# Performance work log

Hardware: AMD Instinct MI355X
Metric: run time of the kernel (lower is better)

## Reference

```python
import jax, jax.numpy as jnp
import numpy as np

N_HEAD, D_MODEL, D_HEAD = 16, 1024, 64
SCALE = 1.0 / (D_HEAD ** 0.5)
LN_EPS = 1e-5


def _rel_shift(x):
    # x: [b, n, i, j] -> Transformer-XL relative shift
    b, n, i, j = x.shape
    zero_pad = jnp.zeros((b, n, i, 1), x.dtype)
    x_padded = jnp.concatenate([zero_pad, x], axis=3).reshape(b, n, j + 1, i)
    return x_padded[:, :, 1:, :].reshape(b, n, i, j)


def setup_inputs() -> dict:
    key = jax.random.key(0)
    ks = jax.random.split(key, 16)
    qlen, bsz, mem_len = 1024, 2, 1024
    klen = qlen + mem_len
    rlen = klen
    s = 0.02
    inp = {
        'w': jax.random.normal(ks[0], (qlen, bsz, D_MODEL), jnp.float32),
        'r': jax.random.normal(ks[1], (rlen, D_MODEL), jnp.float32),
        'mems': jax.random.normal(ks[2], (mem_len, bsz, D_MODEL), jnp.float32),
        'r_w_bias': s * jax.random.normal(ks[3], (N_HEAD, D_HEAD), jnp.float32),
        'r_r_bias': s * jax.random.normal(ks[4], (N_HEAD, D_HEAD), jnp.float32),
        # causal mask with memory offset: position i attends to j <= i + mem_len
        'attn_mask': jnp.triu(jnp.ones((qlen, klen), bool), k=1 + mem_len),
        'Wq': s * jax.random.normal(ks[5], (D_MODEL, N_HEAD * D_HEAD), jnp.float32),
        'bq': jnp.zeros((N_HEAD * D_HEAD,), jnp.float32),
        'Wk': s * jax.random.normal(ks[6], (D_MODEL, N_HEAD * D_HEAD), jnp.float32),
        'bk': jnp.zeros((N_HEAD * D_HEAD,), jnp.float32),
        'Wv': s * jax.random.normal(ks[7], (D_MODEL, N_HEAD * D_HEAD), jnp.float32),
        'bv': jnp.zeros((N_HEAD * D_HEAD,), jnp.float32),
        'Wr': s * jax.random.normal(ks[8], (D_MODEL, N_HEAD * D_HEAD), jnp.float32),
        'br': jnp.zeros((N_HEAD * D_HEAD,), jnp.float32),
        'Wo': s * jax.random.normal(ks[9], (N_HEAD * D_HEAD, D_MODEL), jnp.float32),
        'bo': jnp.zeros((D_MODEL,), jnp.float32),
        'ln_g': jnp.ones((D_MODEL,), jnp.float32),
        'ln_b': jnp.zeros((D_MODEL,), jnp.float32),
    }
    return inp


def reference(w, r, mems, r_w_bias, r_r_bias, Wq, bq, Wk, bk, Wv, bv, Wr, br, Wo, bo, ln_g, ln_b, attn_mask):
    qlen, bsz, _ = w.shape
    cat = jnp.concatenate([mems, w], axis=0)                      # [klen, b, d_model]
    klen = cat.shape[0]
    q = (cat @ Wq + bq)[-qlen:].reshape(qlen, bsz, N_HEAD, D_HEAD)
    k = (cat @ Wk + bk).reshape(klen, bsz, N_HEAD, D_HEAD)
    v = (cat @ Wv + bv).reshape(klen, bsz, N_HEAD, D_HEAD)
    rk = (r @ Wr + br).reshape(-1, N_HEAD, D_HEAD)               # [rlen, n, d]

    AC = jnp.einsum('ibnd,jbnd->bnij', q + r_w_bias, k)          # content term
    BD = _rel_shift(jnp.einsum('ibnd,jnd->bnij', q + r_r_bias, rk))  # relative term
    attn_score = SCALE * (AC + BD)                                # [b, n, i, j]
    attn_score = jnp.where(attn_mask[None, None, :, :], -jnp.inf, attn_score)
    attn_prob = jax.nn.softmax(attn_score, axis=3)
    attn_vec = jnp.einsum('bnij,jbnd->ibnd', attn_prob, v).reshape(qlen, bsz, N_HEAD * D_HEAD)
    attn_out = attn_vec @ Wo + bo

    res = w + attn_out                                            # post-LN (pre_lnorm=False)
    mu = jnp.mean(res, axis=-1, keepdims=True)
    var = jnp.var(res, axis=-1, keepdims=True)
    return (res - mu) / jnp.sqrt(var + LN_EPS) * ln_g + ln_b
```

## Files before the change

### kernel.cpp

```cpp
#include <hip/hip_runtime.h>
#include <math.h>

#define N_HEADC 16
#define D_MODELC 1024
#define D_HEADC 64
#define QLENC 1024
#define BSZC 2
#define MEMLENC 1024
#define KLENC 2048
#define SCALEC 0.125f
#define SL2C 0.18033688011112042f
#define LN_EPSC 1e-5f
#define RINGC 192

typedef __attribute__((ext_vector_type(8))) short short8;
typedef __attribute__((ext_vector_type(4))) float f32x4;

#define MFMA16(a, b, c) __builtin_amdgcn_mfma_f32_16x16x32_bf16((a), (b), (c), 0, 0, 0)

__device__ inline unsigned short f2bf(float x) {
    union { float f; unsigned int u; } c; c.f = x;
    unsigned int r = c.u + 0x7FFFu + ((c.u >> 16) & 1u);
    return (unsigned short)(r >> 16);
}
__device__ inline unsigned int pk2(float a, float b) {
    union { float f; unsigned int u; } x, y; x.f = a; y.f = b;
    return (x.u >> 16) | (y.u & 0xFFFF0000u);
}
__device__ inline float bf2f(short s) {
    union { unsigned int u; float f; } c; c.u = ((unsigned int)(unsigned short)s) << 16;
    return c.f;
}

__device__ __forceinline__ void load_lds16(const short* g, short* l) {
    __builtin_amdgcn_global_load_lds(
        (const __attribute__((address_space(1))) void*)g,
        (__attribute__((address_space(3))) void*)l,
        16, 0, 0);
}

__global__ __launch_bounds__(256) void cast_cat_kernel(
    const float* __restrict__ s0, const float* __restrict__ s1, int splitElems,
    short* __restrict__ dst)
{
    int idx = (blockIdx.x * 256 + threadIdx.x) * 8;
    const float* src = (idx < splitElems) ? (s0 + idx) : (s1 + (idx - splitElems));
    short8 o;
    #pragma unroll
    for (int e = 0; e < 8; ++e) o[e] = (short)f2bf(src[e]);
    *(short8*)(dst + idx) = o;
}

__global__ __launch_bounds__(256) void tcast5_kernel(
    const float* __restrict__ W0, const float* __restrict__ W1,
    const float* __restrict__ W2, const float* __restrict__ W3,
    const float* __restrict__ W4,
    short* __restrict__ D0, short* __restrict__ D1, short* __restrict__ D2,
    short* __restrict__ D3, short* __restrict__ D4)
{
    __shared__ short tile[64][72];
    const float* W; short* D;
    switch (blockIdx.z) {
        case 0: W = W0; D = D0; break;
        case 1: W = W1; D = D1; break;
        case 2: W = W2; D = D2; break;
        case 3: W = W3; D = D3; break;
        default: W = W4; D = D4; break;
    }
    const int t = threadIdx.x;
    const int n0 = blockIdx.x * 64, k0 = blockIdx.y * 64;
    #pragma unroll
    for (int it = 0; it < 2; ++it) {
        int idx = t + it * 256;
        int kl = idx >> 3, c8 = idx & 7;
        const float* src = W + (size_t)(k0 + kl) * D_MODELC + n0 + c8 * 8;
        short8 s;
        #pragma unroll
        for (int e = 0; e < 8; ++e) s[e] = (short)f2bf(src[e]);
        *(short8*)&tile[kl][c8 * 8] = s;
    }
    __syncthreads();
    #pragma unroll
    for (int it = 0; it < 2; ++it) {
        int idx = t + it * 256;
        int nl = idx >> 3, c8 = idx & 7;
        short8 s;
        #pragma unroll
        for (int e = 0; e < 8; ++e) s[e] = tile[c8 * 8 + e][nl];
        *(short8*)(D + (size_t)(n0 + nl) * D_MODELC + k0 + c8 * 8) = s;
    }
}

__global__ __launch_bounds__(256) void vtrans_kernel(
    const short* __restrict__ v_bf, short* __restrict__ vt)
{
    __shared__ short tile[64][72];
    const int t = threadIdx.x;
    const int j0 = blockIdx.x * 64;
    const int bn = blockIdx.y;
    const int b = bn & 1, n = bn >> 1;
    #pragma unroll
    for (int it = 0; it < 2; ++it) {
        int idx = t + it * 256;
        int jl = idx >> 3, c8 = idx & 7;
        short8 s = *(const short8*)(v_bf + ((size_t)(j0 + jl) * 2 + b) * D_MODELC + n * 64 + c8 * 8);
        *(short8*)&tile[jl][c8 * 8] = s;
    }
    __syncthreads();
    #pragma unroll
    for (int it = 0; it < 2; ++it) {
        int idx = t + it * 256;
        int dl = idx >> 3, c8 = idx & 7;
        short8 s;
        #pragma unroll
        for (int e = 0; e < 8; ++e) s[e] = tile[c8 * 8 + e][dl];
        *(short8*)(vt + ((size_t)(b * 16 + n) * 64 + dl) * (size_t)KLENC + j0 + c8 * 8) = s;
    }
}

__global__ __launch_bounds__(256, 3) void proj_gemm_kernel(
    const short* __restrict__ cat, const short* __restrict__ rin,
    const short* __restrict__ WqT, const short* __restrict__ WkT,
    const short* __restrict__ WvT, const short* __restrict__ WrT,
    const float* __restrict__ bq, const float* __restrict__ bk,
    const float* __restrict__ bv, const float* __restrict__ br,
    const float* __restrict__ rwb, const float* __restrict__ rrb,
    short* __restrict__ qw, short* __restrict__ qr,
    short* __restrict__ kb, short* __restrict__ vb, short* __restrict__ rk)
{
    __shared__ short As[128][32];
    __shared__ short Bs[128][32];

    const int lin = blockIdx.y * 8 + blockIdx.x;
    const int sw  = (lin & 7) * 96 + (lin >> 3);
    const int bx  = sw & 7;
    const int by  = sw >> 3;

    const short* A; const short* Bt; const float* bias; int yt, mode;
    if (by < 32)      { A = cat;                         Bt = WkT; bias = bk; yt = by;      mode = 0; }
    else if (by < 64) { A = cat;                         Bt = WvT; bias = bv; yt = by - 32; mode = 1; }
    else if (by < 80) { A = cat + (size_t)2048 * 1024;   Bt = WqT; bias = bq; yt = by - 64; mode = 2; }
    else              { A = rin;                         Bt = WrT; bias = br; yt = by - 80; mode = 3; }

    const int row0 = yt * 128, col0 = bx * 128;
    const int t = threadIdx.x;
    const int lane = t & 63, wid = t >> 6;
    const int row16 = lane & 15, g8 = lane >> 4;
    const int wr = wid >> 1, wc = wid & 1;

    f32x4 acc[4][4];
    #pragma unroll
    for (int m = 0; m < 4; ++m)
        #pragma unroll
        for (int nn = 0; nn < 4; ++nn)
            acc[m][nn] = (f32x4){0.f, 0.f, 0.f, 0.f};

    short* AsB = &As[0][0] + wid * 1024;
    short* BsB = &Bs[0][0] + wid * 1024;
    const int srow4 = lane >> 2;
    const int cs4 = (lane & 3) ^ ((lane >> 3) & 3);
    const short* Ag = A  + (size_t)(row0 + wid * 32 + srow4) * D_MODELC + cs4 * 8;
    const short* Bg = Bt + (size_t)(col0 + wid * 32 + srow4) * D_MODELC + cs4 * 8;
    const int xc2 = (row16 >> 1) & 3;

    for (int k0 = 0; k0 < D_MODELC; k0 += 32) {
        load_lds16(Ag + k0,              AsB);
        load_lds16(Ag + k0 + 16 * 1024,  AsB + 512);
        load_lds16(Bg + k0,              BsB);
        load_lds16(Bg + k0 + 16 * 1024,  BsB + 512);
        __syncthreads();
        short8 af[4], bfr[4];
        #pragma unroll
        for (int m = 0; m < 4; ++m)
            af[m] = *(const short8*)&As[wr * 64 + m * 16 + row16][(g8 ^ xc2) * 8];
        #pragma unroll
        for (int nn = 0; nn < 4; ++nn)
            bfr[nn] = *(const short8*)&Bs[wc * 64 + nn * 16 + row16][(g8 ^ xc2) * 8];
        #pragma unroll
        for (int m = 0; m < 4; ++m)
            #pragma unroll
            for (int nn = 0; nn < 4; ++nn)
                acc[m][nn] = MFMA16(af[m], bfr[nn], acc[m][nn]);
        __syncthreads();
    }

    float bvv[4], w1[4], w2[4];
    #pragma unroll
    for (int nn = 0; nn < 4; ++nn) {
        int c = col0 + wc * 64 + nn * 16 + row16;
        bvv[nn] = bias[c];
        w1[nn] = rwb[c];
        w2[nn] = rrb[c];
    }
    if (mode == 2) {
        #pragma unroll
        for (int m = 0; m < 4; ++m)
            #pragma unroll
            for (int nn = 0; nn < 4; ++nn) {
                int c = col0 + wc * 64 + nn * 16 + row16;
                #pragma unroll
                for (int reg = 0; reg < 4; ++reg) {
                    int r = row0 + wr * 64 + m * 16 + g8 * 4 + reg;
                    float v = acc[m][nn][reg] + bvv[nn];
                    qw[(size_t)r * D_MODELC + c] = (short)f2bf(v + w1[nn]);
                    qr[(size_t)r * D_MODELC + c] = (short)f2bf(v + w2[nn]);
                }
            }
    } else {
        short* C = (mode == 0) ? kb : (mode == 1) ? vb : rk;
        #pragma unroll
        for (int m = 0; m < 4; ++m)
            #pragma unroll
            for (int nn = 0; nn < 4; ++nn) {
                int c = col0 + wc * 64 + nn * 16 + row16;
                #pragma unroll
                for (int reg = 0; reg < 4; ++reg) {
                    int r = row0 + wr * 64 + m * 16 + g8 * 4 + reg;
                    C[(size_t)r * D_MODELC + c] = (short)f2bf(acc[m][nn][reg] + bvv[nn]);
                }
            }
    }
}

__global__ __launch_bounds__(256, 3) void wo_gemm_kernel(
    const short* __restrict__ A, const short* __restrict__ Bt,
    float* __restrict__ out0, float* __restrict__ out1)
{
    __shared__ short As[128][32];
    __shared__ short Bs[128][32];
    const int kz = blockIdx.z;
    float* C = kz ? out1 : out0;
    const int row0 = blockIdx.y * 128, col0 = blockIdx.x * 128;
    const int t = threadIdx.x;
    const int lane = t & 63, wid = t >> 6;
    const int row16 = lane & 15, g8 = lane >> 4;
    const int wr = wid >> 1, wc = wid & 1;

    f32x4 acc[4][4];
    #pragma unroll
    for (int m = 0; m < 4; ++m)
        #pragma unroll
        for (int nn = 0; nn < 4; ++nn)
            acc[m][nn] = (f32x4){0.f, 0.f, 0.f, 0.f};

    short* AsB = &As[0][0] + wid * 1024;
    short* BsB = &Bs[0][0] + wid * 1024;
    const int srow4 = lane >> 2;
    const int cs4 = (lane & 3) ^ ((lane >> 3) & 3);
    const short* Ag = A  + (size_t)(row0 + wid * 32 + srow4) * D_MODELC + cs4 * 8;
    const short* Bg = Bt + (size_t)(col0 + wid * 32 + srow4) * D_MODELC + cs4 * 8;
    const int xc2 = (row16 >> 1) & 3;

    const int kbase = kz * 512;
    for (int k0 = kbase; k0 < kbase + 512; k0 += 32) {
        load_lds16(Ag + k0,             AsB);
        load_lds16(Ag + k0 + 16 * 1024, AsB + 512);
        load_lds16(Bg + k0,             BsB);
        load_lds16(Bg + k0 + 16 * 1024, BsB + 512);
        __syncthreads();
        short8 af[4], bfr[4];
        #pragma unroll
        for (int m = 0; m < 4; ++m)
            af[m] = *(const short8*)&As[wr * 64 + m * 16 + row16][(g8 ^ xc2) * 8];
        #pragma unroll
        for (int nn = 0; nn < 4; ++nn)
            bfr[nn] = *(const short8*)&Bs[wc * 64 + nn * 16 + row16][(g8 ^ xc2) * 8];
        #pragma unroll
        for (int m = 0; m < 4; ++m)
            #pragma unroll
            for (int nn = 0; nn < 4; ++nn)
                acc[m][nn] = MFMA16(af[m], bfr[nn], acc[m][nn]);
        __syncthreads();
    }

    #pragma unroll
    for (int m = 0; m < 4; ++m)
        #pragma unroll
        for (int nn = 0; nn < 4; ++nn) {
            int c = col0 + wc * 64 + nn * 16 + row16;
            #pragma unroll
            for (int reg = 0; reg < 4; ++reg) {
                int r = row0 + wr * 64 + m * 16 + g8 * 4 + reg;
                C[(size_t)r * D_MODELC + c] = acc[m][nn][reg];
            }
        }
}

__global__ __launch_bounds__(256, 2) void attn_mfma_kernel(
    const short* __restrict__ qw, const short* __restrict__ qr,
    const short* __restrict__ kb, const short* __restrict__ rkb,
    const short* __restrict__ vt, short* __restrict__ av)
{
    __shared__ short Kl[2][64][64];
    __shared__ short Vl[2][64][64];
    __shared__ short Rl[RINGC][64];
    __shared__ short pun[4][1376];
    __shared__ float scb[4][16];

    const int wave = threadIdx.x >> 6, lane = threadIdx.x & 63;
    const int row16 = lane & 15, g8 = lane >> 4;
    const int srow = lane >> 3, chk = lane & 7;
    const int swz = srow & 7;

    const int lin = blockIdx.y * 16 + blockIdx.x;
    const int xcd = lin & 7;
    const int u   = lin >> 3;
    const int v   = u & 31;
    const int bn  = xcd * 4 + (v >> 3);
    const int tt  = v & 7;
    const int ic  = (u >> 5) ? (15 - tt) : tt;
    const int b = bn & 1, n = bn >> 1;
    const int i0 = ic * 64;
    const int i0w = i0 + wave * 16;

    short8 qwf[2], qrf[2];
    #pragma unroll
    for (int ks = 0; ks < 2; ++ks) {
        size_t off = ((size_t)(i0w + row16) * 2 + b) * D_MODELC + n * 64 + ks * 32 + g8 * 8;
        qwf[ks] = *(const short8*)(qw + off);
        qrf[ks] = *(const short8*)(qr + off);
    }

    #pragma unroll
    for (int t = 0; t < 2; ++t) {
        int rr = wave * 16 + t * 8;
        int j  = rr + srow;
        int cs = chk ^ swz;
        load_lds16(kb + ((size_t)j * 2 + b) * D_MODELC + n * 64 + cs * 8, &Kl[0][rr][0]);
        load_lds16(vt + ((size_t)((b * 16 + n) * 64 + rr + srow)) * KLENC + cs * 8,
                   &Vl[0][rr][0]);
    }
    {
        const int p0 = 960 - i0;
        #pragma unroll
        for (int t = 0; t < 4; ++t) {
            int jrb_ = p0 + wave * 32 + t * 8;
            int slotb = jrb_ % RINGC;
            int jr = jrb_ + srow;
            int jc = jr < KLENC ? jr : KLENC - 1;
            int cs = chk ^ swz;
            load_lds16(rkb + (size_t)jc * D_MODELC + n * 64 + cs * 8, &Rl[slotb][0]);
        }
    }

    f32x4 accO[4];
    #pragma unroll
    for (int dt = 0; dt < 4; ++dt) accO[dt] = (f32x4){0.f, 0.f, 0.f, 0.f};
    float m = -INFINITY, lsum = 0.f;

    const int T = (i0 + 63 + MEMLENC + 64) >> 6;
    const int r7 = row16 & 7;

    __syncthreads();

    int cur = 0;
    for (int s = 0; s < T; ++s) {
        const int j0 = s * 64;
        const int nxt = cur ^ 1;

        #pragma unroll
        for (int t = 0; t < 2; ++t) {
            int rr = wave * 16 + t * 8;
            int j  = j0 + 64 + rr + srow;
            if (j > KLENC - 1) j = KLENC - 1;
            int cs = chk ^ swz;
            load_lds16(kb + ((size_t)j * 2 + b) * D_MODELC + n * 64 + cs * 8, &Kl[nxt][rr][0]);
        }
        {
            const int nb = j0 + 1088 - i0;
            #pragma unroll
            for (int t = 0; t < 2; ++t) {
                int jrb_ = nb + wave * 16 + t * 8;
                int slotb = jrb_ % RINGC;
                int jr = jrb_ + srow;
                int jc = jr < KLENC ? jr : KLENC - 1;
                int cs = chk ^ swz;
                load_lds16(rkb + (size_t)jc * D_MODELC + n * 64 + cs * 8, &Rl[slotb][0]);
            }
        }
        {
            const int jsrc = (j0 + 64 <= KLENC - 64) ? (j0 + 64) : (KLENC - 64);
            #pragma unroll
            for (int t = 0; t < 2; ++t) {
                int rr = wave * 16 + t * 8;
                int cs = chk ^ swz;
                load_lds16(vt + ((size_t)((b * 16 + n) * 64 + rr + srow)) * KLENC + jsrc + cs * 8,
                           &Vl[nxt][rr][0]);
            }
        }

        __builtin_amdgcn_s_setprio(1);
        f32x4 st[4];
        #pragma unroll
        for (int jt = 0; jt < 4; ++jt) {
            st[jt] = (f32x4){0.f, 0.f, 0.f, 0.f};
            const short* kr = &Kl[cur][jt * 16 + row16][0];
            st[jt] = MFMA16(*(const short8*)(kr + ((g8 ^ r7) * 8)),       qwf[0], st[jt]);
            st[jt] = MFMA16(*(const short8*)(kr + (((4 + g8) ^ r7) * 8)), qwf[1], st[jt]);
        }

        const int jrb_w = j0 - i0w + 1008;
        const int sb = jrb_w % RINGC;
        short* bdT = &pun[wave][0];
        #pragma unroll
        for (int rt = 0; rt < 5; ++rt) {
            int rsl = sb + rt * 16 + row16;
            if (rsl >= RINGC) rsl -= RINGC;
            const short* rr = &Rl[rsl][0];
            f32x4 bd = (f32x4){0.f, 0.f, 0.f, 0.f};
            bd = MFMA16(*(const short8*)(rr + ((g8 ^ r7) * 8)),       qrf[0], bd);
            bd = MFMA16(*(const short8*)(rr + (((4 + g8) ^ r7) * 8)), qrf[1], bd);
            uint2 wv;
            wv.x = pk2(bd[0], bd[1]);
            wv.y = pk2(bd[2], bd[3]);
            *(uint2*)&bdT[row16 * 84 + rt * 16 + g8 * 4] = wv;
        }
        __builtin_amdgcn_s_setprio(0);

        float sl[4][4];
        #pragma unroll
        for (int jt = 0; jt < 4; ++jt)
            #pragma unroll
            for (int reg = 0; reg < 4; ++reg) {
                const int jl = jt * 16 + g8 * 4 + reg;
                float vv = st[jt][reg] + bf2f(bdT[row16 * 84 + jl + 15 - row16]);
                sl[jt][reg] = (j0 + jl > i0w + row16 + MEMLENC) ? -INFINITY : vv * SL2C;
            }

        float mx0 = fmaxf(fmaxf(sl[0][0], sl[0][1]), fmaxf(sl[0][2], sl[0][3]));
        float mx1 = fmaxf(fmaxf(sl[1][0], sl[1][1]), fmaxf(sl[1][2], sl[1][3]));
        float mx2 = fmaxf(fmaxf(sl[2][0], sl[2][1]), fmaxf(sl[2][2], sl[2][3]));
        float mx3 = fmaxf(fmaxf(sl[3][0], sl[3][1]), fmaxf(sl[3][2], sl[3][3]));
        float mx = fmaxf(fmaxf(mx0, mx1), fmaxf(mx2, mx3));
        mx = fmaxf(mx, __shfl_xor(mx, 16, 64));
        mx = fmaxf(mx, __shfl_xor(mx, 32, 64));

        if (__any(mx > m + 8.f)) {
            float mn = fmaxf(m, mx);
            float sc = exp2f(m - mn);
            m = mn;
            lsum *= sc;
            if (lane < 16) scb[wave][lane] = sc;
            float4 s4 = *(const float4*)&scb[wave][g8 * 4];
            #pragma unroll
            for (int dt = 0; dt < 4; ++dt) {
                accO[dt][0] *= s4.x; accO[dt][1] *= s4.y;
                accO[dt][2] *= s4.z; accO[dt][3] *= s4.w;
            }
        }

        float ps = 0.f;
        #pragma unroll
        for (int jt = 0; jt < 4; ++jt)
            #pragma unroll
            for (int reg = 0; reg < 4; ++reg) {
                float p = exp2f(sl[jt][reg] - m);
                sl[jt][reg] = p;
                ps += p;
            }
        short* pP = &pun[wave][0];
        #pragma unroll
        for (int jt = 0; jt < 4; ++jt) {
            const int ch = (jt * 2 + (g8 >> 1)) ^ r7;
            uint2 pkd;
            pkd.x = pk2(sl[jt][0], sl[jt][1]);
            pkd.y = pk2(sl[jt][2], sl[jt][3]);
            *(uint2*)&pP[row16 * 64 + ch * 8 + (g8 & 1) * 4] = pkd;
        }
        ps += __shfl_xor(ps, 16, 64);
        ps += __shfl_xor(ps, 32, 64);
        lsum += ps;

        __builtin_amdgcn_s_setprio(1);
        #pragma unroll
        for (int ks2 = 0; ks2 < 2; ++ks2) {
            short8 pf = *(const short8*)&pP[row16 * 64 + (((ks2 * 4 + g8) ^ r7) * 8)];
            #pragma unroll
            for (int dt = 0; dt < 4; ++dt) {
                const short* vp = &Vl[cur][dt * 16 + row16][(((ks2 * 4 + g8) ^ r7) * 8)];
                accO[dt] = MFMA16(pf, *(const short8*)vp, accO[dt]);
            }
        }
        __builtin_amdgcn_s_setprio(0);

        __syncthreads();
        cur = nxt;
    }

    if (lane < 16) scb[wave][lane] = lsum;
    float4 l4 = *(const float4*)&scb[wave][g8 * 4];
    float rl4[4] = {1.f / l4.x, 1.f / l4.y, 1.f / l4.z, 1.f / l4.w};
    #pragma unroll
    for (int dt = 0; dt < 4; ++dt)
        #pragma unroll
        for (int reg = 0; reg < 4; ++reg) {
            size_t o = ((size_t)(i0w + g8 * 4 + reg) * 2 + b) * D_MODELC + n * 64 + dt * 16 + row16;
            av[o] = (short)f2bf(accO[dt][reg] * rl4[reg]);
        }
}

__global__ __launch_bounds__(256) void ln_kernel(
    const float* __restrict__ w, const float* __restrict__ ao0,
    const float* __restrict__ ao1, const float* __restrict__ bo,
    const float* __restrict__ g, const float* __restrict__ bb,
    float* __restrict__ out)
{
    __shared__ float red[2][4];
    const int row = blockIdx.x;
    const int lane = threadIdx.x & 63;
    const int wv = threadIdx.x >> 6;
    const size_t base = (size_t)row * D_MODELC;
    const int c = threadIdx.x * 4;

    float4 xw = *(const float4*)&w[base + c];
    float4 x0 = *(const float4*)&ao0[base + c];
    float4 x1 = *(const float4*)&ao1[base + c];
    float4 xb = *(const float4*)&bo[c];
    float x[4] = {xw.x + x0.x + x1.x + xb.x, xw.y + x0.y + x1.y + xb.y,
                  xw.z + x0.z + x1.z + xb.z, xw.w + x0.w + x1.w + xb.w};

    float sum = x[0] + x[1] + x[2] + x[3];
    float ssq = x[0]*x[0] + x[1]*x[1] + x[2]*x[2] + x[3]*x[3];
    #pragma unroll
    for (int off = 32; off > 0; off >>= 1) {
        sum += __shfl_xor(sum, off, 64);
        ssq += __shfl_xor(ssq, off, 64);
    }
    if (lane == 0) { red[0][wv] = sum; red[1][wv] = ssq; }
    __syncthreads();
    sum = red[0][0] + red[0][1] + red[0][2] + red[0][3];
    ssq = red[1][0] + red[1][1] + red[1][2] + red[1][3];

    const float mu = sum * (1.0f / D_MODELC);
    const float var = ssq * (1.0f / D_MODELC) - mu * mu;
    const float rstd = rsqrtf(var + LN_EPSC);

    float4 o;
    o.x = (x[0] - mu) * rstd * g[c] + bb[c];
    o.y = (x[1] - mu) * rstd * g[c+1] + bb[c+1];
    o.z = (x[2] - mu) * rstd * g[c+2] + bb[c+2];
    o.w = (x[3] - mu) * rstd * g[c+3] + bb[c+3];
    *(float4*)&out[base + c] = o;
}

extern "C" void kernel_launch(void* const* d_in, const int* in_sizes, int n_in,
                              void* d_out, int out_size, void* d_ws, size_t ws_size,
                              hipStream_t stream)
{
    const float* w    = (const float*)d_in[0];
    const float* r    = (const float*)d_in[1];
    const float* mems = (const float*)d_in[2];
    const float* rwb  = (const float*)d_in[3];
    const float* rrb  = (const float*)d_in[4];
    const float* Wq = (const float*)d_in[6];
    const float* bq = (const float*)d_in[7];
    const float* Wk = (const float*)d_in[8];
    const float* bk = (const float*)d_in[9];
    const float* Wv = (const float*)d_in[10];
    const float* bv = (const float*)d_in[11];
    const float* Wr = (const float*)d_in[12];
    const float* br = (const float*)d_in[13];
    const float* Wo = (const float*)d_in[14];
    const float* bo = (const float*)d_in[15];
    const float* ln_g = (const float*)d_in[16];
    const float* ln_b = (const float*)d_in[17];
    float* out = (float*)d_out;

    char* ws = (char*)d_ws;
    const size_t MB = 1ull << 20;
    short* cat_bf = (short*)(ws + 0 * MB);
    short* r_bf   = (short*)(ws + 8 * MB);
    short* Wq_t   = (short*)(ws + 12 * MB);
    short* Wk_t   = (short*)(ws + 14 * MB);
    short* Wv_t   = (short*)(ws + 16 * MB);
    short* Wr_t   = (short*)(ws + 18 * MB);
    short* Wo_t   = (short*)(ws + 20 * MB);
    short* qw_bf  = (short*)(ws + 22 * MB);
    short* qr_bf  = (short*)(ws + 26 * MB);
    short* k_bf   = (short*)(ws + 30 * MB);
    short* v_bf   = (short*)(ws + 38 * MB);
    short* rk_bf  = (short*)(ws + 46 * MB);
    short* vt     = (short*)(ws + 50 * MB);
    short* av_bf  = (short*)(ws + 58 * MB);
    float* ao0    = (float*)v_bf;
    float* ao1    = (float*)k_bf;

    dim3 blk(256);

    cast_cat_kernel<<<dim3(2048), blk, 0, stream>>>(mems, w, 2048 * 1024, cat_bf);
    cast_cat_kernel<<<dim3(1024), blk, 0, stream>>>(r, r, 1 << 30, r_bf);

    tcast5_kernel<<<dim3(16, 16, 5), blk, 0, stream>>>(
        Wq, Wk, Wv, Wr, Wo, Wq_t, Wk_t, Wv_t, Wr_t, Wo_t);

    proj_gemm_kernel<<<dim3(8, 96), blk, 0, stream>>>(
        cat_bf, r_bf, Wq_t, Wk_t, Wv_t, Wr_t,
        bq, bk, bv, br, rwb, rrb,
        qw_bf, qr_bf, k_bf, v_bf, rk_bf);

    vtrans_kernel<<<dim3(32, 32), blk, 0, stream>>>(v_bf, vt);

    attn_mfma_kernel<<<dim3(16, 32), blk, 0, stream>>>(
        qw_bf, qr_bf, k_bf, rk_bf, vt, av_bf);

    wo_gemm_kernel<<<dim3(8, 16, 2), blk, 0, stream>>>(av_bf, Wo_t, ao0, ao1);

    ln_kernel<<<dim3(2048), blk, 0, stream>>>(w, ao0, ao1, bo, ln_g, ln_b, out);
}
```

Measured before the change: 156.5 us.

## Triple-buffer GEMM k-loops, defer PV matmul, fold softmax scale into Q

The projection and output GEMMs now use a three-stage LDS ring with prefetch two tiles ahead. A vmcnt wait plus a single barrier replaces the two __syncthreads per k-step, and the MFMA block runs at raised priority. The attention kernel adds a third V buffer and software-pipelines P·V: the previous tile's P·V runs while the next tile's scores are computed. It also pre-multiplies Q by the log2 softmax scale in the projection epilogue, and skips masking on tiles that are fully unmasked. The cost is more LDS per block, which may reduce occupancy, and the reordered P/bdT buffer reuse carries some correctness risk.

New measurement: 159.3 us. About the same (+1.8%).

```diff
diff --git a/kernel.cpp b/kernel.cpp
--- a/kernel.cpp
+++ b/kernel.cpp
@@ -128,8 +128,8 @@
     short* __restrict__ qw, short* __restrict__ qr,
     short* __restrict__ kb, short* __restrict__ vb, short* __restrict__ rk)
 {
-    __shared__ short As[128][32];
-    __shared__ short Bs[128][32];
+    __shared__ short As[3][128][32];
+    __shared__ short Bs[3][128][32];
 
     const int lin = blockIdx.y * 8 + blockIdx.x;
     const int sw  = (lin & 7) * 96 + (lin >> 3);
@@ -155,34 +155,51 @@
         for (int nn = 0; nn < 4; ++nn)
             acc[m][nn] = (f32x4){0.f, 0.f, 0.f, 0.f};
 
-    short* AsB = &As[0][0] + wid * 1024;
-    short* BsB = &Bs[0][0] + wid * 1024;
     const int srow4 = lane >> 2;
     const int cs4 = (lane & 3) ^ ((lane >> 3) & 3);
     const short* Ag = A  + (size_t)(row0 + wid * 32 + srow4) * D_MODELC + cs4 * 8;
     const short* Bg = Bt + (size_t)(col0 + wid * 32 + srow4) * D_MODELC + cs4 * 8;
     const int xc2 = (row16 >> 1) & 3;
 
-    for (int k0 = 0; k0 < D_MODELC; k0 += 32) {
-        load_lds16(Ag + k0,              AsB);
-        load_lds16(Ag + k0 + 16 * 1024,  AsB + 512);
-        load_lds16(Bg + k0,              BsB);
-        load_lds16(Bg + k0 + 16 * 1024,  BsB + 512);
-        __syncthreads();
+    #pragma unroll
+    for (int pb = 0; pb < 2; ++pb) {
+        int k0 = pb * 32;
+        load_lds16(Ag + k0,             &As[pb][0][0] + wid * 1024);
+        load_lds16(Ag + k0 + 16 * 1024, &As[pb][0][0] + wid * 1024 + 512);
+        load_lds16(Bg + k0,             &Bs[pb][0][0] + wid * 1024);
+        load_lds16(Bg + k0 + 16 * 1024, &Bs[pb][0][0] + wid * 1024 + 512);
+    }
+    asm volatile("s_waitcnt vmcnt(4)" ::: "memory");
+    __builtin_amdgcn_s_barrier();
+
+    for (int kk = 0; kk < 32; ++kk) {
+        int kpre = (kk + 2 <= 31) ? (kk + 2) * 32 : 31 * 32;
+        int bpre = (kk + 2) % 3;
+        load_lds16(Ag + kpre,             &As[bpre][0][0] + wid * 1024);
+        load_lds16(Ag + kpre + 16 * 1024, &As[bpre][0][0] + wid * 1024 + 512);
+        load_lds16(Bg + kpre,             &Bs[bpre][0][0] + wid * 1024);
+        load_lds16(Bg + kpre + 16 * 1024, &Bs[bpre][0][0] + wid * 1024 + 512);
+
+        const int bc = kk % 3;
         short8 af[4], bfr[4];
         #pragma unroll
         for (int m = 0; m < 4; ++m)
-            af[m] = *(const short8*)&As[wr * 64 + m * 16 + row16][(g8 ^ xc2) * 8];
+            af[m] = *(const short8*)&As[bc][wr * 64 + m * 16 + row16][(g8 ^ xc2) * 8];
         #pragma unroll
         for (int nn = 0; nn < 4; ++nn)
-            bfr[nn] = *(const short8*)&Bs[wc * 64 + nn * 16 + row16][(g8 ^ xc2) * 8];
+            bfr[nn] = *(const short8*)&Bs[bc][wc * 64 + nn * 16 + row16][(g8 ^ xc2) * 8];
+        __builtin_amdgcn_s_setprio(1);
         #pragma unroll
         for (int m = 0; m < 4; ++m)
             #pragma unroll
             for (int nn = 0; nn < 4; ++nn)
                 acc[m][nn] = MFMA16(af[m], bfr[nn], acc[m][nn]);
-        __syncthreads();
-    }
+        __builtin_amdgcn_s_setprio(0);
+
+        asm volatile("s_waitcnt vmcnt(4)" ::: "memory");
+        __builtin_amdgcn_s_barrier();
+    }
+    asm volatile("s_waitcnt vmcnt(0)" ::: "memory");
 
     float bvv[4], w1[4], w2[4];
     #pragma unroll
@@ -202,8 +219,8 @@
                 for (int reg = 0; reg < 4; ++reg) {
                     int r = row0 + wr * 64 + m * 16 + g8 * 4 + reg;
                     float v = acc[m][nn][reg] + bvv[nn];
-                    qw[(size_t)r * D_MODELC + c] = (short)f2bf(v + w1[nn]);
-                    qr[(size_t)r * D_MODELC + c] = (short)f2bf(v + w2[nn]);
+                    qw[(size_t)r * D_MODELC + c] = (short)f2bf((v + w1[nn]) * SL2C);
+                    qr[(size_t)r * D_MODELC + c] = (short)f2bf((v + w2[nn]) * SL2C);
                 }
             }
     } else {
@@ -226,8 +243,8 @@
     const short* __restrict__ A, const short* __restrict__ Bt,
     float* __restrict__ out0, float* __restrict__ out1)
 {
-    __shared__ short As[128][32];
-    __shared__ short Bs[128][32];
+    __shared__ short As[3][128][32];
+    __shared__ short Bs[3][128][32];
     const int kz = blockIdx.z;
     float* C = kz ? out1 : out0;
     const int row0 = blockIdx.y * 128, col0 = blockIdx.x * 128;
@@ -243,35 +260,52 @@
         for (int nn = 0; nn < 4; ++nn)
             acc[m][nn] = (f32x4){0.f, 0.f, 0.f, 0.f};
 
-    short* AsB = &As[0][0] + wid * 1024;
-    short* BsB = &Bs[0][0] + wid * 1024;
     const int srow4 = lane >> 2;
     const int cs4 = (lane & 3) ^ ((lane >> 3) & 3);
-    const short* Ag = A  + (size_t)(row0 + wid * 32 + srow4) * D_MODELC + cs4 * 8;
-    const short* Bg = Bt + (size_t)(col0 + wid * 32 + srow4) * D_MODELC + cs4 * 8;
+    const int kbase = kz * 512;
+    const short* Ag = A  + (size_t)(row0 + wid * 32 + srow4) * D_MODELC + kbase + cs4 * 8;
+    const short* Bg = Bt + (size_t)(col0 + wid * 32 + srow4) * D_MODELC + kbase + cs4 * 8;
     const int xc2 = (row16 >> 1) & 3;
 
-    const int kbase = kz * 512;
-    for (int k0 = kbase; k0 < kbase + 512; k0 += 32) {
-        load_lds16(Ag + k0,             AsB);
-        load_lds16(Ag + k0 + 16 * 1024, AsB + 512);
-        load_lds16(Bg + k0,             BsB);
-        load_lds16(Bg + k0 + 16 * 1024, BsB + 512);
-        __syncthreads();
+    #pragma unroll
+    for (int pb = 0; pb < 2; ++pb) {
+        int k0 = pb * 32;
+        load_lds16(Ag + k0,             &As[pb][0][0] + wid * 1024);
+        load_lds16(Ag + k0 + 16 * 1024, &As[pb][0][0] + wid * 1024 + 512);
+        load_lds16(Bg + k0,             &Bs[pb][0][0] + wid * 1024);
+        load_lds16(Bg + k0 + 16 * 1024, &Bs[pb][0][0] + wid * 1024 + 512);
+    }
+    asm volatile("s_waitcnt vmcnt(4)" ::: "memory");
+    __builtin_amdgcn_s_barrier();
+
+    for (int kk = 0; kk < 16; ++kk) {
+        int kpre = (kk + 2 <= 15) ? (kk + 2) * 32 : 15 * 32;
+        int bpre = (kk + 2) % 3;
+        load_lds16(Ag + kpre,             &As[bpre][0][0] + wid * 1024);
+        load_lds16(Ag + kpre + 16 * 1024, &As[bpre][0][0] + wid * 1024 + 512);
+        load_lds16(Bg + kpre,             &Bs[bpre][0][0] + wid * 1024);
+        load_lds16(Bg + kpre + 16 * 1024, &Bs[bpre][0][0] + wid * 1024 + 512);
+
+        const int bc = kk % 3;
         short8 af[4], bfr[4];
         #pragma unroll
         for (int m = 0; m < 4; ++m)
-            af[m] = *(const short8*)&As[wr * 64 + m * 16 + row16][(g8 ^ xc2) * 8];
+            af[m] = *(const short8*)&As[bc][wr * 64 + m * 16 + row16][(g8 ^ xc2) * 8];
         #pragma unroll
         for (int nn = 0; nn < 4; ++nn)
-            bfr[nn] = *(const short8*)&Bs[wc * 64 + nn * 16 + row16][(g8 ^ xc2) * 8];
+            bfr[nn] = *(const short8*)&Bs[bc][wc * 64 + nn * 16 + row16][(g8 ^ xc2) * 8];
+        __builtin_amdgcn_s_setprio(1);
         #pragma unroll
         for (int m = 0; m < 4; ++m)
             #pragma unroll
             for (int nn = 0; nn < 4; ++nn)
                 acc[m][nn] = MFMA16(af[m], bfr[nn], acc[m][nn]);
-        __syncthreads();
-    }
+        __builtin_amdgcn_s_setprio(0);
+
+        asm volatile("s_waitcnt vmcnt(4)" ::: "memory");
+        __builtin_amdgcn_s_barrier();
+    }
+    asm volatile("s_waitcnt vmcnt(0)" ::: "memory");
 
     #pragma unroll
     for (int m = 0; m < 4; ++m)
@@ -292,7 +326,7 @@
     const short* __restrict__ vt, short* __restrict__ av)
 {
     __shared__ short Kl[2][64][64];
-    __shared__ short Vl[2][64][64];
+    __shared__ short Vl[3][64][64];
     __shared__ short Rl[RINGC][64];
     __shared__ short pun[4][1376];
     __shared__ float scb[4][16];
@@ -354,6 +388,7 @@
     __syncthreads();
 
     int cur = 0;
+    int vp = 2, vc = 0, vn = 1;
     for (int s = 0; s < T; ++s) {
         const int j0 = s * 64;
         const int nxt = cur ^ 1;
@@ -385,9 +420,12 @@
                 int rr = wave * 16 + t * 8;
                 int cs = chk ^ swz;
                 load_lds16(vt + ((size_t)((b * 16 + n) * 64 + rr + srow)) * KLENC + jsrc + cs * 8,
-                           &Vl[nxt][rr][0]);
-            }
-        }
+                           &Vl[vn][rr][0]);
+            }
+        }
+
+        short* pP  = &pun[wave][0];
+        short* bdT = &pun[wave][0];
 
         __builtin_amdgcn_s_setprio(1);
         f32x4 st[4];
@@ -399,9 +437,20 @@
             st[jt] = MFMA16(*(const short8*)(kr + (((4 + g8) ^ r7) * 8)), qwf[1], st[jt]);
         }
 
+        if (s) {
+            #pragma unroll
+            for (int ks2 = 0; ks2 < 2; ++ks2) {
+                short8 pf = *(const short8*)&pP[row16 * 64 + (((ks2 * 4 + g8) ^ r7) * 8)];
+                #pragma unroll
+                for (int dt = 0; dt < 4; ++dt) {
+                    const short* vpp = &Vl[vp][dt * 16 + row16][(((ks2 * 4 + g8) ^ r7) * 8)];
+                    accO[dt] = MFMA16(pf, *(const short8*)vpp, accO[dt]);
+                }
+            }
+        }
+
         const int jrb_w = j0 - i0w + 1008;
         const int sb = jrb_w % RINGC;
-        short* bdT = &pun[wave][0];
         #pragma unroll
         for (int rt = 0; rt < 5; ++rt) {
             int rsl = sb + rt * 16 + row16;
@@ -418,14 +467,24 @@
         __builtin_amdgcn_s_setprio(0);
 
         float sl[4][4];
-        #pragma unroll
-        for (int jt = 0; jt < 4; ++jt)
-            #pragma unroll
-            for (int reg = 0; reg < 4; ++reg) {
-                const int jl = jt * 16 + g8 * 4 + reg;
-                float vv = st[jt][reg] + bf2f(bdT[row16 * 84 + jl + 15 - row16]);
-                sl[jt][reg] = (j0 + jl > i0w + row16 + MEMLENC) ? -INFINITY : vv * SL2C;
-            }
+        if (j0 + 63 <= i0w + MEMLENC) {
+            #pragma unroll
+            for (int jt = 0; jt < 4; ++jt)
+                #pragma unroll
+                for (int reg = 0; reg < 4; ++reg) {
+                    const int jl = jt * 16 + g8 * 4 + reg;
+                    sl[jt][reg] = st[jt][reg] + bf2f(bdT[row16 * 84 + jl + 15 - row16]);
+                }
+        } else {
+            #pragma unroll
+            for (int jt = 0; jt < 4; ++jt)
+                #pragma unroll
+                for (int reg = 0; reg < 4; ++reg) {
+                    const int jl = jt * 16 + g8 * 4 + reg;
+                    float vv = st[jt][reg] + bf2f(bdT[row16 * 84 + jl + 15 - row16]);
+                    sl[jt][reg] = (j0 + jl > i0w + row16 + MEMLENC) ? -INFINITY : vv;
+                }
+        }
 
         float mx0 = fmaxf(fmaxf(sl[0][0], sl[0][1]), fmaxf(sl[0][2], sl[0][3]));
         float mx1 = fmaxf(fmaxf(sl[1][0], sl[1][1]), fmaxf(sl[1][2], sl[1][3]));
@@ -449,16 +508,15 @@
             }
         }
 
-        float ps = 0.f;
         #pragma unroll
         for (int jt = 0; jt < 4; ++jt)
             #pragma unroll
-            for (int reg = 0; reg < 4; ++reg) {
-                float p = exp2f(sl[jt][reg] - m);
-                sl[jt][reg] = p;
-                ps += p;
-            }
-        short* pP = &pun[wave][0];
+            for (int reg = 0; reg < 4; ++reg)
+                sl[jt][reg] = exp2f(sl[jt][reg] - m);
+        float ps = ((sl[0][0] + sl[0][1]) + (sl[0][2] + sl[0][3]))
+                 + ((sl[1][0] + sl[1][1]) + (sl[1][2] + sl[1][3]))
+                 + ((sl[2][0] + sl[2][1]) + (sl[2][2] + sl[2][3]))
+                 + ((sl[3][0] + sl[3][1]) + (sl[3][2] + sl[3][3]));
         #pragma unroll
         for (int jt = 0; jt < 4; ++jt) {
             const int ch = (jt * 2 + (g8 >> 1)) ^ r7;
@@ -471,20 +529,22 @@
         ps += __shfl_xor(ps, 32, 64);
         lsum += ps;
 
-        __builtin_amdgcn_s_setprio(1);
+        __syncthreads();
+        cur = nxt;
+        int tmp = vp; vp = vc; vc = vn; vn = tmp;
+    }
+
+    {
+        short* pP = &pun[wave][0];
         #pragma unroll
         for (int ks2 = 0; ks2 < 2; ++ks2) {
             short8 pf = *(const short8*)&pP[row16 * 64 + (((ks2 * 4 + g8) ^ r7) * 8)];
             #pragma unroll
             for (int dt = 0; dt < 4; ++dt) {
-                const short* vp = &Vl[cur][dt * 16 + row16][(((ks2 * 4 + g8) ^ r7) * 8)];
-                accO[dt] = MFMA16(pf, *(const short8*)vp, accO[dt]);
-            }
-        }
-        __builtin_amdgcn_s_setprio(0);
-
-        __syncthreads();
-        cur = nxt;
+                const short* vpp = &Vl[vp][dt * 16 + row16][(((ks2 * 4 + g8) ^ r7) * 8)];
+                accO[dt] = MFMA16(pf, *(const short8*)vpp, accO[dt]);
+            }
+        }
     }
 
     if (lane < 16) scb[wave][lane] = lsum;
```

## Merge prep casts, fold softmax scale into Q, stream V from global, bf16 Wo partials

Applied to the files above, without the earlier changes.

The three input/weight cast launches become one prep kernel, which cuts launch overhead. The softmax scale is folded into the Q projection epilogue, and masking is skipped for tiles that lie fully in the unmasked region. V fragments are read directly from global memory into registers instead of being staged through LDS. The Wo split-K partials are stored in bf16 to halve their traffic, and setprio is added around the MFMA loops of the GEMMs. These trade some precision (scaled Q in bf16, bf16 partial sums) and global-load latency in the attention loop for less LDS use and less memory traffic.

Measured after the change: 175.2 us. 11.9% more time.

```diff
diff --git a/kernel.cpp b/kernel.cpp
--- a/kernel.cpp
+++ b/kernel.cpp
@@ -39,35 +39,46 @@
         16, 0, 0);
 }
 
-__global__ __launch_bounds__(256) void cast_cat_kernel(
-    const float* __restrict__ s0, const float* __restrict__ s1, int splitElems,
-    short* __restrict__ dst)
-{
-    int idx = (blockIdx.x * 256 + threadIdx.x) * 8;
-    const float* src = (idx < splitElems) ? (s0 + idx) : (s1 + (idx - splitElems));
-    short8 o;
-    #pragma unroll
-    for (int e = 0; e < 8; ++e) o[e] = (short)f2bf(src[e]);
-    *(short8*)(dst + idx) = o;
-}
-
-__global__ __launch_bounds__(256) void tcast5_kernel(
+__global__ __launch_bounds__(256) void prep_kernel(
+    const float* __restrict__ mems, const float* __restrict__ wIn,
+    const float* __restrict__ rIn,
     const float* __restrict__ W0, const float* __restrict__ W1,
     const float* __restrict__ W2, const float* __restrict__ W3,
     const float* __restrict__ W4,
+    short* __restrict__ cat_bf, short* __restrict__ r_bf,
     short* __restrict__ D0, short* __restrict__ D1, short* __restrict__ D2,
     short* __restrict__ D3, short* __restrict__ D4)
 {
     __shared__ short tile[64][72];
+    const int z = blockIdx.z;
+    const int t = threadIdx.x;
+
+    if (z >= 5) {
+        int lb = (z - 5) * 256 + blockIdx.y * 16 + blockIdx.x;
+        int idx = (lb * 256 + t) * 8;
+        const float* src; short* dst;
+        if (idx < 4194304) {
+            src = (idx < 2097152) ? (mems + idx) : (wIn + idx - 2097152);
+            dst = cat_bf + idx;
+        } else {
+            src = rIn + (idx - 4194304);
+            dst = r_bf + (idx - 4194304);
+        }
+        short8 o;
+        #pragma unroll
+        for (int e = 0; e < 8; ++e) o[e] = (short)f2bf(src[e]);
+        *(short8*)dst = o;
+        return;
+    }
+
     const float* W; short* D;
-    switch (blockIdx.z) {
+    switch (z) {
         case 0: W = W0; D = D0; break;
         case 1: W = W1; D = D1; break;
         case 2: W = W2; D = D2; break;
         case 3: W = W3; D = D3; break;
         default: W = W4; D = D4; break;
     }
-    const int t = threadIdx.x;
     const int n0 = blockIdx.x * 64, k0 = blockIdx.y * 64;
     #pragma unroll
     for (int it = 0; it < 2; ++it) {
@@ -176,11 +187,13 @@
         #pragma unroll
         for (int nn = 0; nn < 4; ++nn)
             bfr[nn] = *(const short8*)&Bs[wc * 64 + nn * 16 + row16][(g8 ^ xc2) * 8];
+        __builtin_amdgcn_s_setprio(1);
         #pragma unroll
         for (int m = 0; m < 4; ++m)
             #pragma unroll
             for (int nn = 0; nn < 4; ++nn)
                 acc[m][nn] = MFMA16(af[m], bfr[nn], acc[m][nn]);
+        __builtin_amdgcn_s_setprio(0);
         __syncthreads();
     }
 
@@ -202,8 +215,8 @@
                 for (int reg = 0; reg < 4; ++reg) {
                     int r = row0 + wr * 64 + m * 16 + g8 * 4 + reg;
                     float v = acc[m][nn][reg] + bvv[nn];
-                    qw[(size_t)r * D_MODELC + c] = (short)f2bf(v + w1[nn]);
-                    qr[(size_t)r * D_MODELC + c] = (short)f2bf(v + w2[nn]);
+                    qw[(size_t)r * D_MODELC + c] = (short)f2bf((v + w1[nn]) * SL2C);
+                    qr[(size_t)r * D_MODELC + c] = (short)f2bf((v + w2[nn]) * SL2C);
                 }
             }
     } else {
@@ -224,12 +237,12 @@
 
 __global__ __launch_bounds__(256, 3) void wo_gemm_kernel(
     const short* __restrict__ A, const short* __restrict__ Bt,
-    float* __restrict__ out0, float* __restrict__ out1)
+    short* __restrict__ out0, short* __restrict__ out1)
 {
     __shared__ short As[128][32];
     __shared__ short Bs[128][32];
     const int kz = blockIdx.z;
-    float* C = kz ? out1 : out0;
+    short* C = kz ? out1 : out0;
     const int row0 = blockIdx.y * 128, col0 = blockIdx.x * 128;
     const int t = threadIdx.x;
     const int lane = t & 63, wid = t >> 6;
@@ -251,7 +264,7 @@
     const short* Bg = Bt + (size_t)(col0 + wid * 32 + srow4) * D_MODELC + cs4 * 8;
     const int xc2 = (row16 >> 1) & 3;
 
-    const int kbase = kz * 512;
+    const int kbase = blockIdx.z * 512;
     for (int k0 = kbase; k0 < kbase + 512; k0 += 32) {
         load_lds16(Ag + k0,             AsB);
         load_lds16(Ag + k0 + 16 * 1024, AsB + 512);
@@ -265,11 +278,13 @@
         #pragma unroll
         for (int nn = 0; nn < 4; ++nn)
             bfr[nn] = *(const short8*)&Bs[wc * 64 + nn * 16 + row16][(g8 ^ xc2) * 8];
+        __builtin_amdgcn_s_setprio(1);
         #pragma unroll
         for (int m = 0; m < 4; ++m)
             #pragma unroll
             for (int nn = 0; nn < 4; ++nn)
                 acc[m][nn] = MFMA16(af[m], bfr[nn], acc[m][nn]);
+        __builtin_amdgcn_s_setprio(0);
         __syncthreads();
     }
 
@@ -281,7 +296,7 @@
             #pragma unroll
             for (int reg = 0; reg < 4; ++reg) {
                 int r = row0 + wr * 64 + m * 16 + g8 * 4 + reg;
-                C[(size_t)r * D_MODELC + c] = acc[m][nn][reg];
+                C[(size_t)r * D_MODELC + c] = (short)f2bf(acc[m][nn][reg]);
             }
         }
 }
@@ -292,7 +307,6 @@
     const short* __restrict__ vt, short* __restrict__ av)
 {
     __shared__ short Kl[2][64][64];
-    __shared__ short Vl[2][64][64];
     __shared__ short Rl[RINGC][64];
     __shared__ short pun[4][1376];
     __shared__ float scb[4][16];
@@ -321,14 +335,14 @@
         qrf[ks] = *(const short8*)(qr + off);
     }
 
+    const short* vbase = vt + ((size_t)((b * 16 + n) * 64 + row16)) * KLENC;
+
     #pragma unroll
     for (int t = 0; t < 2; ++t) {
         int rr = wave * 16 + t * 8;
         int j  = rr + srow;
         int cs = chk ^ swz;
         load_lds16(kb + ((size_t)j * 2 + b) * D_MODELC + n * 64 + cs * 8, &Kl[0][rr][0]);
-        load_lds16(vt + ((size_t)((b * 16 + n) * 64 + rr + srow)) * KLENC + cs * 8,
-                   &Vl[0][rr][0]);
     }
     {
         const int p0 = 960 - i0;
@@ -358,6 +372,14 @@
         const int j0 = s * 64;
         const int nxt = cur ^ 1;
 
+        short8 vf[2][4];
+        #pragma unroll
+        for (int ks2 = 0; ks2 < 2; ++ks2)
+            #pragma unroll
+            for (int dt = 0; dt < 4; ++dt)
+                vf[ks2][dt] = *(const short8*)(vbase + (size_t)(dt * 16) * KLENC
+                                               + j0 + ks2 * 32 + g8 * 8);
+
         #pragma unroll
         for (int t = 0; t < 2; ++t) {
             int rr = wave * 16 + t * 8;
@@ -376,16 +398,6 @@
                 int jc = jr < KLENC ? jr : KLENC - 1;
                 int cs = chk ^ swz;
                 load_lds16(rkb + (size_t)jc * D_MODELC + n * 64 + cs * 8, &Rl[slotb][0]);
-            }
-        }
-        {
-            const int jsrc = (j0 + 64 <= KLENC - 64) ? (j0 + 64) : (KLENC - 64);
-            #pragma unroll
-            for (int t = 0; t < 2; ++t) {
-                int rr = wave * 16 + t * 8;
-                int cs = chk ^ swz;
-                load_lds16(vt + ((size_t)((b * 16 + n) * 64 + rr + srow)) * KLENC + jsrc + cs * 8,
-                           &Vl[nxt][rr][0]);
             }
         }
 
@@ -418,14 +430,24 @@
         __builtin_amdgcn_s_setprio(0);
 
         float sl[4][4];
-        #pragma unroll
-        for (int jt = 0; jt < 4; ++jt)
-            #pragma unroll
-            for (int reg = 0; reg < 4; ++reg) {
-                const int jl = jt * 16 + g8 * 4 + reg;
-                float vv = st[jt][reg] + bf2f(bdT[row16 * 84 + jl + 15 - row16]);
-                sl[jt][reg] = (j0 + jl > i0w + row16 + MEMLENC) ? -INFINITY : vv * SL2C;
-            }
+        if (j0 + 63 <= i0w + MEMLENC) {
+            #pragma unroll
+            for (int jt = 0; jt < 4; ++jt)
+                #pragma unroll
+                for (int reg = 0; reg < 4; ++reg) {
+                    const int jl = jt * 16 + g8 * 4 + reg;
+                    sl[jt][reg] = st[jt][reg] + bf2f(bdT[row16 * 84 + jl + 15 - row16]);
+                }
+        } else {
+            #pragma unroll
+            for (int jt = 0; jt < 4; ++jt)
+                #pragma unroll
+                for (int reg = 0; reg < 4; ++reg) {
+                    const int jl = jt * 16 + g8 * 4 + reg;
+                    float vv = st[jt][reg] + bf2f(bdT[row16 * 84 + jl + 15 - row16]);
+                    sl[jt][reg] = (j0 + jl > i0w + row16 + MEMLENC) ? -INFINITY : vv;
+                }
+        }
 
         float mx0 = fmaxf(fmaxf(sl[0][0], sl[0][1]), fmaxf(sl[0][2], sl[0][3]));
         float mx1 = fmaxf(fmaxf(sl[1][0], sl[1][1]), fmaxf(sl[1][2], sl[1][3]));
@@ -449,15 +471,15 @@
             }
         }
 
-        float ps = 0.f;
         #pragma unroll
         for (int jt = 0; jt < 4; ++jt)
             #pragma unroll
-            for (int reg = 0; reg < 4; ++reg) {
-                float p = exp2f(sl[jt][reg] - m);
-                sl[jt][reg] = p;
-                ps += p;
-            }
+            for (int reg = 0; reg < 4; ++reg)
+                sl[jt][reg] = exp2f(sl[jt][reg] - m);
+        float ps = ((sl[0][0] + sl[0][1]) + (sl[0][2] + sl[0][3]))
+                 + ((sl[1][0] + sl[1][1]) + (sl[1][2] + sl[1][3]))
+                 + ((sl[2][0] + sl[2][1]) + (sl[2][2] + sl[2][3]))
+                 + ((sl[3][0] + sl[3][1]) + (sl[3][2] + sl[3][3]));
         short* pP = &pun[wave][0];
         #pragma unroll
         for (int jt = 0; jt < 4; ++jt) {
@@ -476,10 +498,8 @@
         for (int ks2 = 0; ks2 < 2; ++ks2) {
             short8 pf = *(const short8*)&pP[row16 * 64 + (((ks2 * 4 + g8) ^ r7) * 8)];
             #pragma unroll
-            for (int dt = 0; dt < 4; ++dt) {
-                const short* vp = &Vl[cur][dt * 16 + row16][(((ks2 * 4 + g8) ^ r7) * 8)];
-                accO[dt] = MFMA16(pf, *(const short8*)vp, accO[dt]);
-            }
+            for (int dt = 0; dt < 4; ++dt)
+                accO[dt] = MFMA16(pf, vf[ks2][dt], accO[dt]);
         }
         __builtin_amdgcn_s_setprio(0);
 
@@ -500,8 +520,8 @@
 }
 
 __global__ __launch_bounds__(256) void ln_kernel(
-    const float* __restrict__ w, const float* __restrict__ ao0,
-    const float* __restrict__ ao1, const float* __restrict__ bo,
+    const float* __restrict__ w, const short* __restrict__ p0,
+    const short* __restrict__ p1, const float* __restrict__ bo,
     const float* __restrict__ g, const float* __restrict__ bb,
     float* __restrict__ out)
 {
@@ -513,11 +533,13 @@
     const int c = threadIdx.x * 4;
 
     float4 xw = *(const float4*)&w[base + c];
-    float4 x0 = *(const float4*)&ao0[base + c];
-    float4 x1 = *(const float4*)&ao1[base + c];
+    ushort4 a0 = *(const ushort4*)&p0[base + c];
+    ushort4 a1 = *(const ushort4*)&p1[base + c];
     float4 xb = *(const float4*)&bo[c];
-    float x[4] = {xw.x + x0.x + x1.x + xb.x, xw.y + x0.y + x1.y + xb.y,
-                  xw.z + x0.z + x1.z + xb.z, xw.w + x0.w + x1.w + xb.w};
+    float x[4] = {xw.x + bf2f((short)a0.x) + bf2f((short)a1.x) + xb.x,
+                  xw.y + bf2f((short)a0.y) + bf2f((short)a1.y) + xb.y,
+                  xw.z + bf2f((short)a0.z) + bf2f((short)a1.z) + xb.z,
+                  xw.w + bf2f((short)a0.w) + bf2f((short)a1.w) + xb.w};
 
     float sum = x[0] + x[1] + x[2] + x[3];
     float ssq = x[0]*x[0] + x[1]*x[1] + x[2]*x[2] + x[3]*x[3];
@@ -582,16 +604,14 @@
     short* rk_bf  = (short*)(ws + 46 * MB);
     short* vt     = (short*)(ws + 50 * MB);
     short* av_bf  = (short*)(ws + 58 * MB);
-    float* ao0    = (float*)v_bf;
-    float* ao1    = (float*)k_bf;
+    short* wo0    = Wq_t;
+    short* wo1    = Wv_t;
 
     dim3 blk(256);
 
-    cast_cat_kernel<<<dim3(2048), blk, 0, stream>>>(mems, w, 2048 * 1024, cat_bf);
-    cast_cat_kernel<<<dim3(1024), blk, 0, stream>>>(r, r, 1 << 30, r_bf);
-
-    tcast5_kernel<<<dim3(16, 16, 5), blk, 0, stream>>>(
-        Wq, Wk, Wv, Wr, Wo, Wq_t, Wk_t, Wv_t, Wr_t, Wo_t);
+    prep_kernel<<<dim3(16, 16, 17), blk, 0, stream>>>(
+        mems, w, r, Wq, Wk, Wv, Wr, Wo,
+        cat_bf, r_bf, Wq_t, Wk_t, Wv_t, Wr_t, Wo_t);
 
     proj_gemm_kernel<<<dim3(8, 96), blk, 0, stream>>>(
         cat_bf, r_bf, Wq_t, Wk_t, Wv_t, Wr_t,
@@ -603,7 +623,7 @@
     attn_mfma_kernel<<<dim3(16, 32), blk, 0, stream>>>(
         qw_bf, qr_bf, k_bf, rk_bf, vt, av_bf);
 
-    wo_gemm_kernel<<<dim3(8, 16, 2), blk, 0, stream>>>(av_bf, Wo_t, ao0, ao1);
-
-    ln_kernel<<<dim3(2048), blk, 0, stream>>>(w, ao0, ao1, bo, ln_g, ln_b, out);
-}
+    wo_gemm_kernel<<<dim3(8, 16, 2), blk, 0, stream>>>(av_bf, Wo_t, wo0, wo1);
+
+    ln_kernel<<<dim3(2048), blk, 0, stream>>>(w, wo0, wo1, bo, ln_g, ln_b, out);
+}
```
